# Kernel tuning notes

Measured on AMD Instinct MI355X. Metric: run time of the kernel, lower is better.

The kernel has to match this reference:

```python
import jax, jax.numpy as jnp
import numpy as np

D_K = 64  # per-head key dim, used for 1/sqrt(d_k) scaling


def setup_inputs() -> dict:
    key = jax.random.key(0)
    ks = jax.random.split(key, 9)
    B, S, D, H, DK, DV = 2, 4096, 512, 8, 64, 64
    s = 0.02
    return {
        "x": jax.random.normal(ks[0], (B, S, D), dtype=jnp.float32),
        "Wq": jax.random.normal(ks[1], (H, D, DK), dtype=jnp.float32) * s,
        "bq": jax.random.normal(ks[2], (H, DK), dtype=jnp.float32) * s,
        "Wk": jax.random.normal(ks[3], (H, D, DK), dtype=jnp.float32) * s,
        "bk": jax.random.normal(ks[4], (H, DK), dtype=jnp.float32) * s,
        "Wv": jax.random.normal(ks[5], (H, D, DV), dtype=jnp.float32) * s,
        "bv": jax.random.normal(ks[6], (H, DV), dtype=jnp.float32) * s,
        "Wo": jax.random.normal(ks[7], (H * DV, D), dtype=jnp.float32) * s,
        "bo": jax.random.normal(ks[8], (D,), dtype=jnp.float32) * s,
    }


def reference(x, Wq, bq, Wk, bk, Wv, bv, Wo, bo):
    # Per-head projections, vectorized over heads: [B,H,S,dk/dv]
    q = jnp.einsum("bsd,hdk->bhsk", x, Wq) + bq[None, :, None, :]
    k = jnp.einsum("bsd,hdk->bhsk", x, Wk) + bk[None, :, None, :]
    v = jnp.einsum("bsd,hdv->bhsv", x, Wv) + bv[None, :, None, :]
    # Scaled dot-product attention (no mask; dropout inactive at eval)
    scores = jnp.einsum("bhsk,bhtk->bhst", q, k) / jnp.sqrt(jnp.float32(D_K))
    attn = jax.nn.softmax(scores, axis=-1)
    o = jnp.einsum("bhst,bhtv->bhsv", attn, v)
    # Concat heads along feature dim: [B,S,H*dv]
    B, H, S, DV = o.shape
    concat = jnp.transpose(o, (0, 2, 1, 3)).reshape(B, S, H * DV)
    return concat @ Wo + bo
```

## Files before the change

kernel.cpp:

```cpp
#include <hip/hip_runtime.h>
#include <hip/hip_bf16.h>

typedef __attribute__((ext_vector_type(8))) short bf16x8;
typedef __attribute__((ext_vector_type(4))) float f32x4;
typedef __attribute__((ext_vector_type(16))) float f32x16;
typedef __attribute__((ext_vector_type(4))) unsigned short u16x4;
typedef __attribute__((ext_vector_type(4))) unsigned int u32x4;

#define NB 2
#define NS 4096
#define ND 512
#define NH 8

__device__ __forceinline__ unsigned short f2bf(float f) {
  unsigned int u = __float_as_uint(f);
  u += 0x7fffu + ((u >> 16) & 1u);
  return (unsigned short)(u >> 16);
}

__device__ __forceinline__ float exp2_hw(float x) {
  float r;
  asm("v_exp_f32 %0, %1" : "=v"(r) : "v"(x));
  return r;
}

__device__ __forceinline__ unsigned cvtpk(float lo, float hi) {
  unsigned r;
  asm("v_cvt_pk_bf16_f32 %0, %1, %2" : "=v"(r) : "v"(lo), "v"(hi));
  return r;
}

__device__ __forceinline__ void swap32(unsigned& a, unsigned& b) {
  asm("v_permlane32_swap_b32 %0, %1" : "+v"(a), "+v"(b));
}

__device__ __forceinline__ bf16x8 mkfrag(unsigned w0, unsigned w1,
                                         unsigned w2, unsigned w3) {
  u32x4 u = {w0, w1, w2, w3};
  return __builtin_bit_cast(bf16x8, u);
}

__device__ __forceinline__ void gload_lds16(const unsigned short* g,
                                            unsigned short* l) {
  __builtin_amdgcn_global_load_lds(
      (const __attribute__((address_space(1))) unsigned int*)g,
      (__attribute__((address_space(3))) unsigned int*)l, 16, 0, 0);
}

__global__ void pack_kernel(const float* __restrict__ x,
                            const float* __restrict__ Wq,
                            const float* __restrict__ Wk,
                            const float* __restrict__ Wv,
                            const float* __restrict__ Wo,
                            unsigned short* __restrict__ x_bf,
                            unsigned short* __restrict__ w3,
                            unsigned short* __restrict__ wo_t)
{
  int idx = blockIdx.x * 256 + threadIdx.x;
  const int NX4 = NB * NS * ND / 4;
  const int NW = 512 * 512;
  if (idx < NX4) {
    const float4 f = ((const float4*)x)[idx];
    u16x4 o;
    o[0] = f2bf(f.x); o[1] = f2bf(f.y); o[2] = f2bf(f.z); o[3] = f2bf(f.w);
    ((u16x4*)x_bf)[idx] = o;
  } else if (idx < NX4 + 3 * NW) {
    int j = idx - NX4;
    int p = j / NW;
    int r = j - p * NW;
    int n = r >> 9, d = r & 511;
    int h = n >> 6, o = n & 63;
    const float* W = (p == 0) ? Wq : (p == 1) ? Wk : Wv;
    w3[j] = f2bf(W[(h * 512 + d) * 64 + o]);
  } else if (idx < NX4 + 4 * NW) {
    int j = idx - NX4 - 3 * NW;
    int n = j >> 9, kk = j & 511;
    wo_t[j] = f2bf(Wo[kk * 512 + n]);
  }
}

template <int MODE>
__global__ __launch_bounds__(256, 2) void gemm_bt(
    const unsigned short* __restrict__ A,
    const unsigned short* __restrict__ Bm,
    const float* __restrict__ b0,
    const float* __restrict__ b1,
    const float* __restrict__ b2,
    unsigned short* __restrict__ qo,
    unsigned short* __restrict__ ko,
    unsigned short* __restrict__ vo,
    float* __restrict__ fo) {
  __shared__ unsigned short Al[2][128 * 32];
  __shared__ unsigned short Bl[2][128 * 32];
  const int t = threadIdx.x;
  const int m0 = blockIdx.x * 128;
  const int n0 = blockIdx.y * 128;
  const int lane = t & 63;
  const int w = t >> 6;
  const int wm = w >> 1, wn = w & 1;
  const int c = lane & 15, g = lane >> 4;

  f32x4 acc[4][4];
#pragma unroll
  for (int i = 0; i < 4; ++i)
#pragma unroll
    for (int j = 0; j < 4; ++j) acc[i][j] = (f32x4){0.f, 0.f, 0.f, 0.f};

  const int rr = lane >> 2;
  const int kc = (lane & 3) * 8;
  const unsigned short* Ab = A + (size_t)(m0 + w * 32 + rr) * 512 + kc;
  const unsigned short* Bb = Bm + (size_t)(n0 + w * 32 + rr) * 512 + kc;

  auto ISSUE = [&](int ks, int bi) {
    const int k0 = ks * 32;
    gload_lds16(Ab + k0, &Al[bi][w * 1024]);
    gload_lds16(Ab + 16 * 512 + k0, &Al[bi][w * 1024 + 512]);
    gload_lds16(Bb + k0, &Bl[bi][w * 1024]);
    gload_lds16(Bb + 16 * 512 + k0, &Bl[bi][w * 1024 + 512]);
  };

  ISSUE(0, 0);
  for (int ks = 0; ks < 16; ++ks) {
    const int cur = ks & 1;
    asm volatile("s_waitcnt vmcnt(0)" ::: "memory");
    __builtin_amdgcn_s_barrier();
    __builtin_amdgcn_sched_barrier(0);
    if (ks + 1 < 16) ISSUE(ks + 1, cur ^ 1);

    bf16x8 af[4], bfr[4];
#pragma unroll
    for (int mf = 0; mf < 4; ++mf)
      af[mf] = *(const bf16x8*)&Al[cur][(wm * 64 + mf * 16 + c) * 32 + g * 8];
#pragma unroll
    for (int nf = 0; nf < 4; ++nf)
      bfr[nf] = *(const bf16x8*)&Bl[cur][(wn * 64 + nf * 16 + c) * 32 + g * 8];
    __builtin_amdgcn_s_setprio(1);
#pragma unroll
    for (int mf = 0; mf < 4; ++mf)
#pragma unroll
      for (int nf = 0; nf < 4; ++nf)
        acc[mf][nf] = __builtin_amdgcn_mfma_f32_16x16x32_bf16(
            af[mf], bfr[nf], acc[mf][nf], 0, 0, 0);
    __builtin_amdgcn_s_setprio(0);
  }

  if (MODE == 0) {
    const int proj = n0 >> 9;
    const float* bias = proj == 0 ? b0 : (proj == 1 ? b1 : b2);
    unsigned short* dst01 = proj == 0 ? qo : ko;
    const float scale = proj == 0 ? 0.18033688011112042f : 1.0f;
#pragma unroll
    for (int nf = 0; nf < 4; ++nf) {
      const int col5 = (n0 + wn * 64 + nf * 16 + c) & 511;
      const int h = col5 >> 6, o = col5 & 63;
      const float bb = bias[col5];
#pragma unroll
      for (int mf = 0; mf < 4; ++mf) {
#pragma unroll
        for (int r = 0; r < 4; ++r) {
          const int m = m0 + wm * 64 + mf * 16 + g * 4 + r;
          const int b = m >> 12, s = m & 4095;
          const unsigned short hb = f2bf((acc[mf][nf][r] + bb) * scale);
          if (proj < 2)
            dst01[((size_t)((b * NH + h) * NS + s)) * 64 + o] = hb;
          else
            vo[((size_t)((b * NH + h) * 64 + o)) * NS + s] = hb;
        }
      }
    }
  } else {
#pragma unroll
    for (int nf = 0; nf < 4; ++nf) {
      const int col = n0 + wn * 64 + nf * 16 + c;
      const float bb = b0[col];
#pragma unroll
      for (int mf = 0; mf < 4; ++mf) {
#pragma unroll
        for (int r = 0; r < 4; ++r) {
          const int m = m0 + wm * 64 + mf * 16 + g * 4 + r;
          fo[(size_t)m * 512 + col] = acc[mf][nf][r] + bb;
        }
      }
    }
  }
}

__global__ __launch_bounds__(256, 2) void attn_kernel(
    const unsigned short* __restrict__ q,
    const unsigned short* __restrict__ k,
    const unsigned short* __restrict__ vt,
    unsigned short* __restrict__ cc)
{
  union SMemU {
    struct { unsigned short Kl[3][4096]; unsigned short Vl[3][4096]; } kv;
    unsigned short Ol[4][32][68];
  };
  __shared__ SMemU sm;
  const int t = threadIdx.x;
  const int w = t >> 6, lane = t & 63;
  const int col = lane & 31, hi = lane >> 5;
  const int bh = blockIdx.y;
  const int b = bh >> 3, h = bh & 7;
  const int q0 = blockIdx.x * 128 + w * 32;

  const unsigned short* qh = q + (size_t)bh * NS * 64;
  const unsigned short* kh = k + (size_t)bh * NS * 64;
  const unsigned short* vh = vt + (size_t)bh * 64 * NS;

  bf16x8 qf[4];
#pragma unroll
  for (int c = 0; c < 4; ++c)
    qf[c] = *(const bf16x8*)&qh[(size_t)(q0 + col) * 64 + c * 16 + hi * 8];

  const int rl = lane >> 3, chn = lane & 7;
  const int lk = rl * 64 + ((chn ^ (rl & 7)) << 3);
  const int lv = rl * NS + ((chn ^ (rl & 7)) << 3);

  auto ISSUE = [&](int tile, int bi) {
    const unsigned short* gk = kh + (size_t)(tile * 64 + w * 16) * 64;
    const unsigned short* gv = vh + (size_t)(w * 16) * NS + tile * 64;
    gload_lds16(gk + lk, &sm.kv.Kl[bi][w * 1024]);
    gload_lds16(gk + lk + 512, &sm.kv.Kl[bi][w * 1024 + 512]);
    gload_lds16(gv + lv, &sm.kv.Vl[bi][w * 1024]);
    gload_lds16(gv + lv + 8 * NS, &sm.kv.Vl[bi][w * 1024 + 512]);
  };

  f32x16 ot0, ot1;
#pragma unroll
  for (int r = 0; r < 16; ++r) { ot0[r] = 0.f; ot1[r] = 0.f; }
  float l_ = 0.f;

  const int NT = NS / 64;

  ISSUE(0, 0);
  ISSUE(1, 1);
  asm volatile("s_waitcnt vmcnt(4)" ::: "memory");
  __builtin_amdgcn_s_barrier();
  __builtin_amdgcn_sched_barrier(0);

  f32x16 p0, p1;
  {
    bf16x8 kfr0[4], kfr1[4];
#pragma unroll
    for (int c = 0; c < 4; ++c) {
      const int cidx = (((2 * c + hi) ^ (col & 7)) << 3);
      kfr0[c] = *(const bf16x8*)&sm.kv.Kl[0][col * 64 + cidx];
      kfr1[c] = *(const bf16x8*)&sm.kv.Kl[0][(col + 32) * 64 + cidx];
    }
#pragma unroll
    for (int r = 0; r < 16; ++r) { p0[r] = 0.f; p1[r] = 0.f; }
    __builtin_amdgcn_s_setprio(1);
#pragma unroll
    for (int c = 0; c < 4; ++c) {
      p0 = __builtin_amdgcn_mfma_f32_32x32x16_bf16(kfr0[c], qf[c], p0, 0, 0, 0);
      p1 = __builtin_amdgcn_mfma_f32_32x32x16_bf16(kfr1[c], qf[c], p1, 0, 0, 0);
    }
    __builtin_amdgcn_s_setprio(0);
  }

  for (int it = 0; it < NT; ++it) {
    const int cur = it - (it / 3) * 3;
    const int nxt = (cur + 1 == 3) ? 0 : cur + 1;

    bf16x8 vfr[2][4];
#pragma unroll
    for (int ks = 0; ks < 4; ++ks) {
      const int cidx = (((2 * ks + hi) ^ (col & 7)) << 3);
      vfr[0][ks] = *(const bf16x8*)&sm.kv.Vl[cur][col * 64 + cidx];
      vfr[1][ks] = *(const bf16x8*)&sm.kv.Vl[cur][(col + 32) * 64 + cidx];
    }

#pragma unroll
    for (int r = 0; r < 16; ++r) {
      p0[r] = exp2_hw(p0[r]);
      p1[r] = exp2_hw(p1[r]);
    }
    {
      float s[8];
#pragma unroll
      for (int r = 0; r < 8; ++r)
        s[r] = (p0[r] + p0[r + 8]) + (p1[r] + p1[r + 8]);
      float rs =
          ((s[0] + s[1]) + (s[2] + s[3])) + ((s[4] + s[5]) + (s[6] + s[7]));
      rs += __shfl_xor(rs, 32, 64);
      l_ += rs;
    }
    bf16x8 pb[4];
    {
      unsigned g0[8], g1[8];
#pragma unroll
      for (int gg = 0; gg < 8; ++gg) {
        g0[gg] = cvtpk(p0[2 * gg], p0[2 * gg + 1]);
        g1[gg] = cvtpk(p1[2 * gg], p1[2 * gg + 1]);
      }
      unsigned a1, b1, c1, d1;
      a1 = g0[0]; b1 = g0[2]; swap32(a1, b1);
      c1 = g0[1]; d1 = g0[3]; swap32(c1, d1);
      pb[0] = mkfrag(a1, c1, b1, d1);
      a1 = g0[4]; b1 = g0[6]; swap32(a1, b1);
      c1 = g0[5]; d1 = g0[7]; swap32(c1, d1);
      pb[1] = mkfrag(a1, c1, b1, d1);
      a1 = g1[0]; b1 = g1[2]; swap32(a1, b1);
      c1 = g1[1]; d1 = g1[3]; swap32(c1, d1);
      pb[2] = mkfrag(a1, c1, b1, d1);
      a1 = g1[4]; b1 = g1[6]; swap32(a1, b1);
      c1 = g1[5]; d1 = g1[7]; swap32(c1, d1);
      pb[3] = mkfrag(a1, c1, b1, d1);
    }

    if (it + 1 < NT) {
      asm volatile("s_waitcnt vmcnt(0)" ::: "memory");
      __builtin_amdgcn_s_barrier();
      __builtin_amdgcn_sched_barrier(0);
      const int b2 = (nxt + 1 == 3) ? 0 : nxt + 1;
      if (it + 2 < NT) ISSUE(it + 2, b2);

      bf16x8 kfr0[4], kfr1[4];
#pragma unroll
      for (int c = 0; c < 4; ++c) {
        const int cidx = (((2 * c + hi) ^ (col & 7)) << 3);
        kfr0[c] = *(const bf16x8*)&sm.kv.Kl[nxt][col * 64 + cidx];
        kfr1[c] = *(const bf16x8*)&sm.kv.Kl[nxt][(col + 32) * 64 + cidx];
      }
#pragma unroll
      for (int r = 0; r < 16; ++r) { p0[r] = 0.f; p1[r] = 0.f; }
      __builtin_amdgcn_s_setprio(1);
#pragma unroll
      for (int c = 0; c < 4; ++c) {
        p0 = __builtin_amdgcn_mfma_f32_32x32x16_bf16(kfr0[c], qf[c], p0, 0, 0, 0);
        p1 = __builtin_amdgcn_mfma_f32_32x32x16_bf16(kfr1[c], qf[c], p1, 0, 0, 0);
      }
#pragma unroll
      for (int ks = 0; ks < 4; ++ks) {
        ot0 = __builtin_amdgcn_mfma_f32_32x32x16_bf16(vfr[0][ks], pb[ks], ot0, 0, 0, 0);
        ot1 = __builtin_amdgcn_mfma_f32_32x32x16_bf16(vfr[1][ks], pb[ks], ot1, 0, 0, 0);
      }
      __builtin_amdgcn_s_setprio(0);
    } else {
      __builtin_amdgcn_s_setprio(1);
#pragma unroll
      for (int ks = 0; ks < 4; ++ks) {
        ot0 = __builtin_amdgcn_mfma_f32_32x32x16_bf16(vfr[0][ks], pb[ks], ot0, 0, 0, 0);
        ot1 = __builtin_amdgcn_mfma_f32_32x32x16_bf16(vfr[1][ks], pb[ks], ot1, 0, 0, 0);
      }
      __builtin_amdgcn_s_setprio(0);
    }
  }

  __syncthreads();

  const float inv = 1.0f / l_;
#pragma unroll
  for (int r = 0; r < 16; ++r) {
    const int dvb = (r & 3) + 8 * (r >> 2) + 4 * hi;
    sm.Ol[w][col][dvb] = f2bf(ot0[r] * inv);
    sm.Ol[w][col][dvb + 32] = f2bf(ot1[r] * inv);
  }
  asm volatile("s_waitcnt lgkmcnt(0)" ::: "memory");
  const int row = lane >> 1;
#pragma unroll
  for (int p = 0; p < 4; ++p) {
    const int chunk = (lane & 1) + 2 * p;
    bf16x8 vv = *(const bf16x8*)&sm.Ol[w][row][chunk * 8];
    *(bf16x8*)&cc[((size_t)(b * NS + q0 + row)) * 512 + h * 64 + chunk * 8] = vv;
  }
}

extern "C" void kernel_launch(void* const* d_in, const int* in_sizes, int n_in,
                              void* d_out, int out_size, void* d_ws, size_t ws_size,
                              hipStream_t stream) {
  const float* x  = (const float*)d_in[0];
  const float* Wq = (const float*)d_in[1];
  const float* bq = (const float*)d_in[2];
  const float* Wk = (const float*)d_in[3];
  const float* bk = (const float*)d_in[4];
  const float* Wv = (const float*)d_in[5];
  const float* bv = (const float*)d_in[6];
  const float* Wo = (const float*)d_in[7];
  const float* bo = (const float*)d_in[8];

  unsigned char* ws = (unsigned char*)d_ws;
  unsigned short* x_bf = (unsigned short*)(ws);
  unsigned short* w3   = (unsigned short*)(ws + 8388608);
  unsigned short* wo_t = (unsigned short*)(ws + 9961472);
  unsigned short* qb   = (unsigned short*)(ws + 10485760);
  unsigned short* kb   = (unsigned short*)(ws + 18874368);
  unsigned short* vb   = (unsigned short*)(ws + 27262976);
  unsigned short* cc   = x_bf;

  pack_kernel<<<8192, 256, 0, stream>>>(x, Wq, Wk, Wv, Wo, x_bf, w3, wo_t);
  gemm_bt<0><<<dim3(64, 12), 256, 0, stream>>>(x_bf, w3, bq, bk, bv, qb, kb, vb,
                                               nullptr);
  attn_kernel<<<dim3(32, 16), 256, 0, stream>>>(qb, kb, vb, cc);
  gemm_bt<1><<<dim3(64, 4), 256, 0, stream>>>(cc, wo_t, bo, nullptr, nullptr,
                                              nullptr, nullptr, nullptr,
                                              (float*)d_out);
}
```

Before: 136.7 us.

## Replace triple-buffered software-pipelined attention loop with simple double buffering

The attention inner loop moves from a 3-stage K/V LDS ring, where the next tile's QK^T MFMAs were interleaved with the current PV MFMAs, to a plain 2-stage double buffer. Each iteration now waits for the current tile, issues the next load, computes QK^T, applies the softmax exponent and runs PV. This cuts LDS use from 48KB to 32KB and simplifies the code, which may help occupancy or register pressure. It gives up the overlap of QK^T with the previous PV and exposes more load latency, since the prefetch distance drops to one tile.

New measurement: 135.8 us. No clear change (-0.7%).

```diff
diff --git a/kernel.cpp b/kernel.cpp
--- a/kernel.cpp
+++ b/kernel.cpp
@@ -192,7 +192,7 @@
     unsigned short* __restrict__ cc)
 {
   union SMemU {
-    struct { unsigned short Kl[3][4096]; unsigned short Vl[3][4096]; } kv;
+    struct { unsigned short Kl[2][4096]; unsigned short Vl[2][4096]; } kv;
     unsigned short Ol[4][32][68];
   };
   __shared__ SMemU sm;
@@ -233,34 +233,31 @@
   const int NT = NS / 64;
 
   ISSUE(0, 0);
-  ISSUE(1, 1);
-  asm volatile("s_waitcnt vmcnt(4)" ::: "memory");
-  __builtin_amdgcn_s_barrier();
-  __builtin_amdgcn_sched_barrier(0);
-
-  f32x16 p0, p1;
-  {
-    bf16x8 kfr0[4], kfr1[4];
+
+  for (int it = 0; it < NT; ++it) {
+    const int cur = it & 1;
+    asm volatile("s_waitcnt vmcnt(0)" ::: "memory");
+    __builtin_amdgcn_s_barrier();
+    __builtin_amdgcn_sched_barrier(0);
+    if (it + 1 < NT) ISSUE(it + 1, cur ^ 1);
+
+    bf16x8 kfr[2][4];
 #pragma unroll
     for (int c = 0; c < 4; ++c) {
       const int cidx = (((2 * c + hi) ^ (col & 7)) << 3);
-      kfr0[c] = *(const bf16x8*)&sm.kv.Kl[0][col * 64 + cidx];
-      kfr1[c] = *(const bf16x8*)&sm.kv.Kl[0][(col + 32) * 64 + cidx];
-    }
+      kfr[0][c] = *(const bf16x8*)&sm.kv.Kl[cur][col * 64 + cidx];
+      kfr[1][c] = *(const bf16x8*)&sm.kv.Kl[cur][(col + 32) * 64 + cidx];
+    }
+    f32x16 p0, p1;
 #pragma unroll
     for (int r = 0; r < 16; ++r) { p0[r] = 0.f; p1[r] = 0.f; }
     __builtin_amdgcn_s_setprio(1);
 #pragma unroll
     for (int c = 0; c < 4; ++c) {
-      p0 = __builtin_amdgcn_mfma_f32_32x32x16_bf16(kfr0[c], qf[c], p0, 0, 0, 0);
-      p1 = __builtin_amdgcn_mfma_f32_32x32x16_bf16(kfr1[c], qf[c], p1, 0, 0, 0);
+      p0 = __builtin_amdgcn_mfma_f32_32x32x16_bf16(kfr[0][c], qf[c], p0, 0, 0, 0);
+      p1 = __builtin_amdgcn_mfma_f32_32x32x16_bf16(kfr[1][c], qf[c], p1, 0, 0, 0);
     }
     __builtin_amdgcn_s_setprio(0);
-  }
-
-  for (int it = 0; it < NT; ++it) {
-    const int cur = it - (it / 3) * 3;
-    const int nxt = (cur + 1 == 3) ? 0 : cur + 1;
 
     bf16x8 vfr[2][4];
 #pragma unroll
@@ -308,43 +305,13 @@
       pb[3] = mkfrag(a1, c1, b1, d1);
     }
 
-    if (it + 1 < NT) {
-      asm volatile("s_waitcnt vmcnt(0)" ::: "memory");
-      __builtin_amdgcn_s_barrier();
-      __builtin_amdgcn_sched_barrier(0);
-      const int b2 = (nxt + 1 == 3) ? 0 : nxt + 1;
-      if (it + 2 < NT) ISSUE(it + 2, b2);
-
-      bf16x8 kfr0[4], kfr1[4];
-#pragma unroll
-      for (int c = 0; c < 4; ++c) {
-        const int cidx = (((2 * c + hi) ^ (col & 7)) << 3);
-        kfr0[c] = *(const bf16x8*)&sm.kv.Kl[nxt][col * 64 + cidx];
-        kfr1[c] = *(const bf16x8*)&sm.kv.Kl[nxt][(col + 32) * 64 + cidx];
-      }
-#pragma unroll
-      for (int r = 0; r < 16; ++r) { p0[r] = 0.f; p1[r] = 0.f; }
-      __builtin_amdgcn_s_setprio(1);
-#pragma unroll
-      for (int c = 0; c < 4; ++c) {
-        p0 = __builtin_amdgcn_mfma_f32_32x32x16_bf16(kfr0[c], qf[c], p0, 0, 0, 0);
-        p1 = __builtin_amdgcn_mfma_f32_32x32x16_bf16(kfr1[c], qf[c], p1, 0, 0, 0);
-      }
-#pragma unroll
-      for (int ks = 0; ks < 4; ++ks) {
-        ot0 = __builtin_amdgcn_mfma_f32_32x32x16_bf16(vfr[0][ks], pb[ks], ot0, 0, 0, 0);
-        ot1 = __builtin_amdgcn_mfma_f32_32x32x16_bf16(vfr[1][ks], pb[ks], ot1, 0, 0, 0);
-      }
-      __builtin_amdgcn_s_setprio(0);
-    } else {
-      __builtin_amdgcn_s_setprio(1);
-#pragma unroll
-      for (int ks = 0; ks < 4; ++ks) {
-        ot0 = __builtin_amdgcn_mfma_f32_32x32x16_bf16(vfr[0][ks], pb[ks], ot0, 0, 0, 0);
-        ot1 = __builtin_amdgcn_mfma_f32_32x32x16_bf16(vfr[1][ks], pb[ks], ot1, 0, 0, 0);
-      }
-      __builtin_amdgcn_s_setprio(0);
-    }
+    __builtin_amdgcn_s_setprio(1);
+#pragma unroll
+    for (int ks = 0; ks < 4; ++ks) {
+      ot0 = __builtin_amdgcn_mfma_f32_32x32x16_bf16(vfr[0][ks], pb[ks], ot0, 0, 0, 0);
+      ot1 = __builtin_amdgcn_mfma_f32_32x32x16_bf16(vfr[1][ks], pb[ks], ot1, 0, 0, 0);
+    }
+    __builtin_amdgcn_s_setprio(0);
   }
 
   __syncthreads();
```
